# Kernel optimization log

Hardware: AMD Instinct MI355X
Metric: run time of the kernel (lower is better)

The kernel has to match this reference:

```python
import jax, jax.numpy as jnp
import numpy as np

B, DIN, H, DOUT, NC = 1024, 343, 512, 311, 4


def cubic(y0, y1, y2, y3, mu):
    # Catmull-Rom cubic interpolation (matches PFNN.cubic)
    return ((-0.5 * y0 + 1.5 * y1 - 1.5 * y2 + 0.5 * y3) * mu * mu * mu
            + (y0 - 2.5 * y1 + 2.0 * y2 - 0.5 * y3) * mu * mu
            + (-0.5 * y0 + 0.5 * y2) * mu + y1)


def setup_inputs() -> dict:
    key = jax.random.key(0)
    ks = jax.random.split(key, 7)
    s = 0.05
    x = jax.random.uniform(ks[0], (B, DIN), dtype=jnp.float32)  # phase = x[:, -1] in [0,1)
    W0 = jax.random.normal(ks[1], (NC, H, DIN - 1), dtype=jnp.float32) * s
    W1 = jax.random.normal(ks[2], (NC, H, H), dtype=jnp.float32) * s
    W2 = jax.random.normal(ks[3], (NC, DOUT, H), dtype=jnp.float32) * s
    b0 = jax.random.normal(ks[4], (NC, H), dtype=jnp.float32) * s
    b1 = jax.random.normal(ks[5], (NC, H), dtype=jnp.float32) * s
    b2 = jax.random.normal(ks[6], (NC, DOUT), dtype=jnp.float32) * s
    return {"x": x, "W0": W0, "W1": W1, "W2": W2, "b0": b0, "b1": b1, "b2": b2}


def reference(x, W0, W1, W2, b0, b1, b2):
    nc = W0.shape[0]
    phase = x[:, -1]                       # [B]
    pscale = nc * phase
    mu = jnp.mod(pscale, 1.0)              # [B]
    k1 = jnp.mod(pscale.astype(jnp.int32), nc)
    k0 = jnp.mod(k1 - 1, nc)
    k2 = jnp.mod(k1 + 1, nc)
    k3 = jnp.mod(k1 + 2, nc)
    muW = mu[:, None, None]
    mub = mu[:, None]

    def interp(P, m):
        return cubic(P[k0], P[k1], P[k2], P[k3], m)

    W0i = interp(W0, muW)  # [B, 512, DIN-1]
    W1i = interp(W1, muW)  # [B, 512, 512]
    W2i = interp(W2, muW)  # [B, DOUT, 512]
    b0i = interp(b0, mub)
    b1i = interp(b1, mub)
    b2i = interp(b2, mub)

    h0 = x[:, :-1]                                              # [B, DIN-1]
    h1 = jax.nn.elu(jnp.einsum('boi,bi->bo', W0i, h0) + b0i)    # [B, 512]
    h2 = jax.nn.elu(jnp.einsum('boi,bi->bo', W1i, h1) + b1i)    # [B, 512]
    h3 = jnp.einsum('boi,bi->bo', W2i, h2) + b2i                # [B, DOUT]
    return h3
```

## Files before the change

kernel.cpp:

```cpp
#include <hip/hip_runtime.h>
#include <math.h>

typedef short bf16x8 __attribute__((ext_vector_type(8)));
typedef float f32x16 __attribute__((ext_vector_type(16)));

__device__ __forceinline__ unsigned short f2bf(float f) {
    union { float f; unsigned u; } x; x.f = f;
    unsigned r = x.u + 0x7FFFu + ((x.u >> 16) & 1u);
    return (unsigned short)(r >> 16);
}


__global__ __launch_bounds__(256) void prep_kernel(
    const float* __restrict__ x, float* __restrict__ coef,
    unsigned short* __restrict__ xb, unsigned short* __restrict__ H1b,
    unsigned short* __restrict__ H2b)
{
    const int b = blockIdx.x, t = threadIdx.x;
    for (int k = t; k < 384; k += 256) {
        unsigned short v;
        if (k < 342)       v = f2bf(x[b * 343 + k]);
        else if (k == 342) v = 0x3F80;
        else               v = 0;
        xb[b * 384 + k] = v;
    }
    if (t >= 64 && t < 128) {
        int j = t - 64;
        H1b[b * 576 + 512 + j] = (j == 0) ? 0x3F80 : 0;
    }
    if (t >= 128 && t < 192) {
        int j = t - 128;
        H2b[b * 576 + 512 + j] = (j == 0) ? 0x3F80 : 0;
    }
    if (t == 0) {
        float phase = x[b * 343 + 342];
        float ps = 4.0f * phase;
        int k1 = (int)ps;
        float mu = ps - (float)k1;
        k1 &= 3;
        float mu2 = mu * mu, mu3 = mu2 * mu;
        float c0 = -0.5f * mu3 +        mu2 - 0.5f * mu;
        float c1 =  1.5f * mu3 - 2.5f * mu2 + 1.0f;
        float c2 = -1.5f * mu3 + 2.0f * mu2 + 0.5f * mu;
        float c3 =  0.5f * mu3 - 0.5f * mu2;
        float cc[4];
        cc[(k1 + 3) & 3] = c0;
        cc[k1]           = c1;
        cc[(k1 + 1) & 3] = c2;
        cc[(k1 + 2) & 3] = c3;
        *(float4*)(coef + b * 4) = make_float4(cc[0], cc[1], cc[2], cc[3]);
    }
}

__global__ __launch_bounds__(256) void convw_kernel(
    const float* __restrict__ W0, const float* __restrict__ W1, const float* __restrict__ W2,
    const float* __restrict__ b0, const float* __restrict__ b1, const float* __restrict__ b2,
    unsigned short* __restrict__ Wf0, unsigned short* __restrict__ Wf1, unsigned short* __restrict__ Wf2)
{
    constexpr unsigned E0 = 4u * 512 * 384;
    constexpr unsigned E1 = 4u * 512 * 576;
    constexpr unsigned E2 = 4u * 320 * 576;
    unsigned i = (blockIdx.x * 256u + threadIdx.x) * 4u;
    if (i >= E0 + E1 + E2) return;
    float v[4];
    unsigned n, o, k, NOT, NKS, KPv;
    unsigned short* dst;
    if (i < E0) {
        n = i / (512u * 384u); unsigned r = i % (512u * 384u);
        o = r / 384u; k = r % 384u; NOT = 16; NKS = 24; KPv = 384; dst = Wf0;
        unsigned row = n * 512u + o;
        #pragma unroll
        for (int j = 0; j < 4; ++j) {
            unsigned kk = k + j;
            v[j] = (kk < 342u) ? W0[(size_t)row * 342u + kk] : ((kk == 342u) ? b0[row] : 0.f);
        }
    } else if (i < E0 + E1) {
        unsigned ii = i - E0;
        n = ii / (512u * 576u); unsigned r = ii % (512u * 576u);
        o = r / 576u; k = r % 576u; NOT = 16; NKS = 36; KPv = 576; dst = Wf1;
        unsigned row = n * 512u + o;
        if (k + 3u < 512u) {
            float4 w = *(const float4*)(W1 + (size_t)row * 512u + k);
            v[0] = w.x; v[1] = w.y; v[2] = w.z; v[3] = w.w;
        } else {
            #pragma unroll
            for (int j = 0; j < 4; ++j) {
                unsigned kk = k + j;
                v[j] = (kk < 512u) ? W1[(size_t)row * 512u + kk] : ((kk == 512u) ? b1[row] : 0.f);
            }
        }
    } else {
        unsigned ii = i - E0 - E1;
        n = ii / (320u * 576u); unsigned r = ii % (320u * 576u);
        o = r / 576u; k = r % 576u; NOT = 10; NKS = 36; KPv = 576; dst = Wf2;
        v[0] = v[1] = v[2] = v[3] = 0.f;
        if (o < 311u) {
            unsigned row = n * 311u + o;
            if (k + 3u < 512u) {
                float4 w = *(const float4*)(W2 + (size_t)row * 512u + k);
                v[0] = w.x; v[1] = w.y; v[2] = w.z; v[3] = w.w;
            } else {
                #pragma unroll
                for (int j = 0; j < 4; ++j) {
                    unsigned kk = k + j;
                    v[j] = (kk < 512u) ? W2[(size_t)row * 512u + kk] : ((kk == 512u) ? b2[row] : 0.f);
                }
            }
        }
    }
    (void)KPv;
    unsigned ot = o >> 5, m = o & 31, ks = k >> 4, h = (k >> 3) & 1, j4 = k & 7;
    size_t off = (((size_t)(n * NOT + ot) * NKS + ks) * 64u + h * 32u + m) * 8u + j4;
    ushort4 pk; pk.x = f2bf(v[0]); pk.y = f2bf(v[1]); pk.z = f2bf(v[2]); pk.w = f2bf(v[3]);
    *(ushort4*)(dst + off) = pk;
}

template<bool ELU, bool OUT_BF16, int KP, int OPAD>
__global__ __launch_bounds__(256) void layer_mfma(
    const unsigned short* __restrict__ Wf,
    const unsigned short* __restrict__ Hb,
    const float* __restrict__ coef,
    unsigned short* __restrict__ HoutB,
    float* __restrict__ outF,
    int Oreal)
{
    constexpr int NOT = OPAD / 32, NKS = KP / 16, KSQ = NKS / 4, RS = KP + 8;
    __shared__ unsigned short hs[32 * RS];

    const int tid = threadIdx.x, lane = tid & 63, w = tid >> 6;
    const int ot = blockIdx.x, b0 = blockIdx.y * 32;

    constexpr int CPT = (32 * KP / 8) / 256;
    #pragma unroll
    for (int c = 0; c < CPT; ++c) {
        int idx = c * 256 + tid;
        int r = idx / (KP / 8), col = idx % (KP / 8);
        *(bf16x8*)&hs[r * RS + col * 8] = *(const bf16x8*)(Hb + (size_t)(b0 + r) * KP + col * 8);
    }
    __syncthreads();

    const int m = lane & 31, h = lane >> 5;
    const unsigned short* hrow = &hs[m * RS + h * 8 + w * KSQ * 16];
    const unsigned short* wbase = Wf + (size_t)ot * NKS * 512 + (size_t)w * KSQ * 512 + lane * 8;
    const size_t nstr = (size_t)NOT * NKS * 512;

    f32x16 acc0 = {}, acc1 = {}, acc2 = {}, acc3 = {};
    #pragma unroll
    for (int s = 0; s < KSQ; ++s) {
        bf16x8 bfr = *(const bf16x8*)(hrow + s * 16);
        bf16x8 a0 = *(const bf16x8*)(wbase + (size_t)s * 512);
        bf16x8 a1 = *(const bf16x8*)(wbase + nstr + (size_t)s * 512);
        bf16x8 a2 = *(const bf16x8*)(wbase + 2 * nstr + (size_t)s * 512);
        bf16x8 a3 = *(const bf16x8*)(wbase + 3 * nstr + (size_t)s * 512);
        acc0 = __builtin_amdgcn_mfma_f32_32x32x16_bf16(a0, bfr, acc0, 0, 0, 0);
        acc1 = __builtin_amdgcn_mfma_f32_32x32x16_bf16(a1, bfr, acc1, 0, 0, 0);
        acc2 = __builtin_amdgcn_mfma_f32_32x32x16_bf16(a2, bfr, acc2, 0, 0, 0);
        acc3 = __builtin_amdgcn_mfma_f32_32x32x16_bf16(a3, bfr, acc3, 0, 0, 0);
    }

    const int b = b0 + m;
    float4 cf = *(const float4*)(coef + b * 4);
    float sv[16];
    #pragma unroll
    for (int r = 0; r < 16; ++r)
        sv[r] = cf.x * acc0[r] + cf.y * acc1[r] + cf.z * acc2[r] + cf.w * acc3[r];

    __syncthreads();
    float* red = (float*)hs;
    if (w > 0) {
        #pragma unroll
        for (int g = 0; g < 4; ++g)
            #pragma unroll
            for (int j = 0; j < 4; ++j) {
                int row = 8 * g + 4 * h + j;
                red[(w - 1) * 1024 + row * 32 + m] = sv[g * 4 + j];
            }
    }
    __syncthreads();
    if (w == 0) {
        #pragma unroll
        for (int g = 0; g < 4; ++g) {
            float vv[4];
            #pragma unroll
            for (int j = 0; j < 4; ++j) {
                int row = 8 * g + 4 * h + j;
                float v = sv[g * 4 + j] + red[row * 32 + m]
                        + red[1024 + row * 32 + m] + red[2048 + row * 32 + m];
                if (ELU) v = (v > 0.f) ? v : expm1f(v);
                vv[j] = v;
            }
            int orow = ot * 32 + 8 * g + 4 * h;
            if (OUT_BF16) {
                ushort4 pk;
                pk.x = f2bf(vv[0]); pk.y = f2bf(vv[1]); pk.z = f2bf(vv[2]); pk.w = f2bf(vv[3]);
                *(ushort4*)(HoutB + (size_t)b * 576 + orow) = pk;
            } else {
                #pragma unroll
                for (int j = 0; j < 4; ++j)
                    if (orow + j < Oreal) outF[(size_t)b * Oreal + orow + j] = vv[j];
            }
        }
    }
}

extern "C" void kernel_launch(void* const* d_in, const int* in_sizes, int n_in,
                              void* d_out, int out_size, void* d_ws, size_t ws_size,
                              hipStream_t stream) {
    (void)in_sizes; (void)n_in; (void)out_size; (void)ws_size;
    const float* x  = (const float*)d_in[0];
    const float* W0 = (const float*)d_in[1];
    const float* W1 = (const float*)d_in[2];
    const float* W2 = (const float*)d_in[3];
    const float* b0 = (const float*)d_in[4];
    const float* b1 = (const float*)d_in[5];
    const float* b2 = (const float*)d_in[6];
    float* out = (float*)d_out;

    char* wsb = (char*)d_ws;
    float*          coef = (float*)(wsb + 0);
    unsigned short* xb   = (unsigned short*)(wsb + 16384);
    unsigned short* H1b  = (unsigned short*)(wsb + 802816);
    unsigned short* H2b  = (unsigned short*)(wsb + 1982464);
    unsigned short* Wf0  = (unsigned short*)(wsb + 3162112);
    unsigned short* Wf1  = (unsigned short*)(wsb + 4734976);
    unsigned short* Wf2  = (unsigned short*)(wsb + 7094272);

    prep_kernel<<<dim3(1024), dim3(256), 0, stream>>>(x, coef, xb, H1b, H2b);
    convw_kernel<<<dim3(2640), dim3(256), 0, stream>>>(W0, W1, W2, b0, b1, b2, Wf0, Wf1, Wf2);

    layer_mfma<true,  true,  384, 512><<<dim3(16, 32), dim3(256), 0, stream>>>(Wf0, xb,  coef, H1b, nullptr, 512);
    layer_mfma<true,  true,  576, 512><<<dim3(16, 32), dim3(256), 0, stream>>>(Wf1, H1b, coef, H2b, nullptr, 512);
    layer_mfma<false, false, 576, 320><<<dim3(10, 32), dim3(256), 0, stream>>>(Wf2, H2b, coef, nullptr, out, 311);
}
```

Baseline: 106.3 us.

## Fuse prep, weight conversion and three layers into one cooperative persistent kernel

Replaces five separate launches with a single cooperative kernel that runs input and weight conversion, then each layer, separated by grid-wide syncs. Activations are now stored directly in MFMA fragment order, so the layers read B operands from global memory without staging them in LDS. Weight conversion writes eight bf16 values per thread in fragment order. The intent is to remove launch gaps and LDS staging, at the cost of grid.sync overhead and a fixed grid of 256 or 512 blocks looping over tiles, with a multi-kernel fallback if the cooperative launch fails.

```diff
diff --git a/kernel.cpp b/kernel.cpp
--- a/kernel.cpp
+++ b/kernel.cpp
@@ -1,5 +1,8 @@
 #include <hip/hip_runtime.h>
+#include <hip/hip_cooperative_groups.h>
 #include <math.h>
+
+namespace cg = cooperative_groups;
 
 typedef short bf16x8 __attribute__((ext_vector_type(8)));
 typedef float f32x16 __attribute__((ext_vector_type(16)));
@@ -10,30 +13,33 @@
     return (unsigned short)(r >> 16);
 }
 
-
-__global__ __launch_bounds__(256) void prep_kernel(
-    const float* __restrict__ x, float* __restrict__ coef,
-    unsigned short* __restrict__ xb, unsigned short* __restrict__ H1b,
-    unsigned short* __restrict__ H2b)
+__device__ __forceinline__ bf16x8 conv8(const float* __restrict__ W,
+                                        const float* __restrict__ bias,
+                                        int row, int Kreal, int k0) {
+    bf16x8 r;
+    #pragma unroll
+    for (int j = 0; j < 8; ++j) {
+        int k = k0 + j;
+        float v = (k < Kreal) ? W[(size_t)row * Kreal + k]
+                              : ((k == Kreal) ? bias[row] : 0.f);
+        r[j] = (short)f2bf(v);
+    }
+    return r;
+}
+
+__device__ void phaseA(
+    const float* __restrict__ x,
+    const float* __restrict__ W0, const float* __restrict__ W1, const float* __restrict__ W2,
+    const float* __restrict__ bias0, const float* __restrict__ bias1, const float* __restrict__ bias2,
+    float* __restrict__ coef, unsigned short* __restrict__ xf,
+    unsigned short* __restrict__ H1f, unsigned short* __restrict__ H2f,
+    unsigned short* __restrict__ Wf0, unsigned short* __restrict__ Wf1, unsigned short* __restrict__ Wf2,
+    int bid, int tid, unsigned gsz)
 {
-    const int b = blockIdx.x, t = threadIdx.x;
-    for (int k = t; k < 384; k += 256) {
-        unsigned short v;
-        if (k < 342)       v = f2bf(x[b * 343 + k]);
-        else if (k == 342) v = 0x3F80;
-        else               v = 0;
-        xb[b * 384 + k] = v;
-    }
-    if (t >= 64 && t < 128) {
-        int j = t - 64;
-        H1b[b * 576 + 512 + j] = (j == 0) ? 0x3F80 : 0;
-    }
-    if (t >= 128 && t < 192) {
-        int j = t - 128;
-        H2b[b * 576 + 512 + j] = (j == 0) ? 0x3F80 : 0;
-    }
-    if (t == 0) {
-        float phase = x[b * 343 + 342];
+    unsigned gtid = (unsigned)bid * 256u + (unsigned)tid;
+
+    for (unsigned b = gtid; b < 1024u; b += gsz) {
+        float phase = x[b * 343u + 342u];
         float ps = 4.0f * phase;
         int k1 = (int)ps;
         float mu = ps - (float)k1;
@@ -50,157 +56,196 @@
         cc[(k1 + 2) & 3] = c3;
         *(float4*)(coef + b * 4) = make_float4(cc[0], cc[1], cc[2], cc[3]);
     }
-}
-
-__global__ __launch_bounds__(256) void convw_kernel(
-    const float* __restrict__ W0, const float* __restrict__ W1, const float* __restrict__ W2,
-    const float* __restrict__ b0, const float* __restrict__ b1, const float* __restrict__ b2,
-    unsigned short* __restrict__ Wf0, unsigned short* __restrict__ Wf1, unsigned short* __restrict__ Wf2)
-{
-    constexpr unsigned E0 = 4u * 512 * 384;
-    constexpr unsigned E1 = 4u * 512 * 576;
-    constexpr unsigned E2 = 4u * 320 * 576;
-    unsigned i = (blockIdx.x * 256u + threadIdx.x) * 4u;
-    if (i >= E0 + E1 + E2) return;
-    float v[4];
-    unsigned n, o, k, NOT, NKS, KPv;
-    unsigned short* dst;
-    if (i < E0) {
-        n = i / (512u * 384u); unsigned r = i % (512u * 384u);
-        o = r / 384u; k = r % 384u; NOT = 16; NKS = 24; KPv = 384; dst = Wf0;
-        unsigned row = n * 512u + o;
-        #pragma unroll
-        for (int j = 0; j < 4; ++j) {
-            unsigned kk = k + j;
-            v[j] = (kk < 342u) ? W0[(size_t)row * 342u + kk] : ((kk == 342u) ? b0[row] : 0.f);
-        }
-    } else if (i < E0 + E1) {
-        unsigned ii = i - E0;
-        n = ii / (512u * 576u); unsigned r = ii % (512u * 576u);
-        o = r / 576u; k = r % 576u; NOT = 16; NKS = 36; KPv = 576; dst = Wf1;
-        unsigned row = n * 512u + o;
-        if (k + 3u < 512u) {
-            float4 w = *(const float4*)(W1 + (size_t)row * 512u + k);
-            v[0] = w.x; v[1] = w.y; v[2] = w.z; v[3] = w.w;
+
+    for (unsigned c = gtid; c < 32u * 24u * 64u; c += gsz) {
+        unsigned lane = c & 63u, r = c >> 6;
+        unsigned ks = r % 24u, bt = r / 24u;
+        int b  = (int)(bt * 32u + (lane & 31u));
+        int k0 = (int)(ks * 16u + (lane >> 5) * 8u);
+        bf16x8 v;
+        #pragma unroll
+        for (int j = 0; j < 8; ++j) {
+            int k = k0 + j;
+            unsigned short s;
+            if (k < 342)       s = f2bf(x[(size_t)b * 343 + k]);
+            else if (k == 342) s = 0x3F80;
+            else               s = 0;
+            v[j] = (short)s;
+        }
+        *(bf16x8*)(xf + (size_t)c * 8) = v;
+    }
+
+    for (unsigned c = gtid; c < 32u * 4u * 64u; c += gsz) {
+        unsigned lane = c & 63u, r = c >> 6;
+        unsigned kk = r & 3u, bt = r >> 2;
+        size_t off = ((size_t)(bt * 36u + 32u + kk) * 64u + lane) * 8u;
+        bf16x8 v;
+        #pragma unroll
+        for (int j = 0; j < 8; ++j)
+            v[j] = (short)((kk == 0u && (lane >> 5) == 0u && j == 0) ? 0x3F80 : 0);
+        *(bf16x8*)(H1f + off) = v;
+        *(bf16x8*)(H2f + off) = v;
+    }
+
+    constexpr unsigned C0 = 4u * 16 * 24 * 64;
+    constexpr unsigned C1 = 4u * 16 * 36 * 64;
+    constexpr unsigned C2 = 4u * 10 * 36 * 64;
+    for (unsigned c = gtid; c < C0 + C1 + C2; c += gsz) {
+        bf16x8 v;
+        unsigned short* dst;
+        if (c < C0) {
+            unsigned lane = c & 63u, r = c >> 6, ks = r % 24u, t = r / 24u;
+            int o  = (int)((t & 15u) * 32u + (lane & 31u));
+            int k0 = (int)(ks * 16u + (lane >> 5) * 8u);
+            v = conv8(W0, bias0, (int)(t >> 4) * 512 + o, 342, k0);
+            dst = Wf0 + (size_t)c * 8;
+        } else if (c < C0 + C1) {
+            unsigned cc = c - C0;
+            unsigned lane = cc & 63u, r = cc >> 6, ks = r % 36u, t = r / 36u;
+            int o  = (int)((t & 15u) * 32u + (lane & 31u));
+            int k0 = (int)(ks * 16u + (lane >> 5) * 8u);
+            v = conv8(W1, bias1, (int)(t >> 4) * 512 + o, 512, k0);
+            dst = Wf1 + (size_t)cc * 8;
         } else {
-            #pragma unroll
-            for (int j = 0; j < 4; ++j) {
-                unsigned kk = k + j;
-                v[j] = (kk < 512u) ? W1[(size_t)row * 512u + kk] : ((kk == 512u) ? b1[row] : 0.f);
-            }
-        }
-    } else {
-        unsigned ii = i - E0 - E1;
-        n = ii / (320u * 576u); unsigned r = ii % (320u * 576u);
-        o = r / 576u; k = r % 576u; NOT = 10; NKS = 36; KPv = 576; dst = Wf2;
-        v[0] = v[1] = v[2] = v[3] = 0.f;
-        if (o < 311u) {
-            unsigned row = n * 311u + o;
-            if (k + 3u < 512u) {
-                float4 w = *(const float4*)(W2 + (size_t)row * 512u + k);
-                v[0] = w.x; v[1] = w.y; v[2] = w.z; v[3] = w.w;
+            unsigned cc = c - C0 - C1;
+            unsigned lane = cc & 63u, r = cc >> 6, ks = r % 36u, t = r / 36u;
+            unsigned ot = t % 10u, n = t / 10u;
+            int o  = (int)(ot * 32u + (lane & 31u));
+            int k0 = (int)(ks * 16u + (lane >> 5) * 8u);
+            if (o < 311) {
+                v = conv8(W2, bias2, (int)n * 311 + o, 512, k0);
             } else {
                 #pragma unroll
+                for (int j = 0; j < 8; ++j) v[j] = 0;
+            }
+            dst = Wf2 + (size_t)cc * 8;
+        }
+        *(bf16x8*)dst = v;
+    }
+}
+
+template<bool ELU, bool OUT_BF16, int KP, int OPAD>
+__device__ __forceinline__ void layer_phase(
+    const unsigned short* __restrict__ Wf,
+    const unsigned short* __restrict__ Hf,
+    const float* __restrict__ coef,
+    unsigned short* __restrict__ HoutF,
+    float* __restrict__ outF, int Oreal,
+    float* red, int bid, int tid, int gdim)
+{
+    constexpr int NOT = OPAD / 32, NKS = KP / 16, KSQ = NKS / 4;
+    const int lane = tid & 63, w = tid >> 6;
+    const int m = lane & 31, h = lane >> 5;
+    const size_t nstr = (size_t)NOT * NKS * 512;
+
+    for (int t = bid; t < NOT * 32; t += gdim) {
+        const int ot = t >> 5, bt = t & 31;
+        const unsigned short* wbase = Wf + ((size_t)ot * NKS + w * KSQ) * 512 + (size_t)lane * 8;
+        const unsigned short* bbase = Hf + ((size_t)bt * NKS + w * KSQ) * 512 + (size_t)lane * 8;
+
+        f32x16 acc0 = {}, acc1 = {}, acc2 = {}, acc3 = {};
+        #pragma unroll
+        for (int s = 0; s < KSQ; ++s) {
+            bf16x8 bfr = *(const bf16x8*)(bbase + (size_t)s * 512);
+            bf16x8 a0 = *(const bf16x8*)(wbase + (size_t)s * 512);
+            bf16x8 a1 = *(const bf16x8*)(wbase + nstr + (size_t)s * 512);
+            bf16x8 a2 = *(const bf16x8*)(wbase + 2 * nstr + (size_t)s * 512);
+            bf16x8 a3 = *(const bf16x8*)(wbase + 3 * nstr + (size_t)s * 512);
+            acc0 = __builtin_amdgcn_mfma_f32_32x32x16_bf16(a0, bfr, acc0, 0, 0, 0);
+            acc1 = __builtin_amdgcn_mfma_f32_32x32x16_bf16(a1, bfr, acc1, 0, 0, 0);
+            acc2 = __builtin_amdgcn_mfma_f32_32x32x16_bf16(a2, bfr, acc2, 0, 0, 0);
+            acc3 = __builtin_amdgcn_mfma_f32_32x32x16_bf16(a3, bfr, acc3, 0, 0, 0);
+        }
+
+        const int b = bt * 32 + m;
+        float4 cf = *(const float4*)(coef + b * 4);
+        float sv[16];
+        #pragma unroll
+        for (int r = 0; r < 16; ++r)
+            sv[r] = cf.x * acc0[r] + cf.y * acc1[r] + cf.z * acc2[r] + cf.w * acc3[r];
+
+        __syncthreads();
+        if (w > 0) {
+            #pragma unroll
+            for (int g = 0; g < 4; ++g)
+                #pragma unroll
                 for (int j = 0; j < 4; ++j) {
-                    unsigned kk = k + j;
-                    v[j] = (kk < 512u) ? W2[(size_t)row * 512u + kk] : ((kk == 512u) ? b2[row] : 0.f);
+                    int row = 8 * g + 4 * h + j;
+                    red[(w - 1) * 1024 + row * 32 + m] = sv[g * 4 + j];
+                }
+        }
+        __syncthreads();
+        if (w == 0) {
+            #pragma unroll
+            for (int g = 0; g < 4; ++g) {
+                float vv[4];
+                #pragma unroll
+                for (int j = 0; j < 4; ++j) {
+                    int row = 8 * g + 4 * h + j;
+                    float v = sv[g * 4 + j] + red[row * 32 + m]
+                            + red[1024 + row * 32 + m] + red[2048 + row * 32 + m];
+                    if (ELU) v = (v > 0.f) ? v : expm1f(v);
+                    vv[j] = v;
+                }
+                if (OUT_BF16) {
+                    size_t off = (((size_t)bt * 36 + ot * 2 + (g >> 1)) * 64
+                                  + (g & 1) * 32 + m) * 8 + 4 * h;
+                    ushort4 pk;
+                    pk.x = f2bf(vv[0]); pk.y = f2bf(vv[1]); pk.z = f2bf(vv[2]); pk.w = f2bf(vv[3]);
+                    *(ushort4*)(HoutF + off) = pk;
+                } else {
+                    int orow = ot * 32 + 8 * g + 4 * h;
+                    #pragma unroll
+                    for (int j = 0; j < 4; ++j)
+                        if (orow + j < Oreal) outF[(size_t)b * Oreal + orow + j] = vv[j];
                 }
             }
         }
     }
-    (void)KPv;
-    unsigned ot = o >> 5, m = o & 31, ks = k >> 4, h = (k >> 3) & 1, j4 = k & 7;
-    size_t off = (((size_t)(n * NOT + ot) * NKS + ks) * 64u + h * 32u + m) * 8u + j4;
-    ushort4 pk; pk.x = f2bf(v[0]); pk.y = f2bf(v[1]); pk.z = f2bf(v[2]); pk.w = f2bf(v[3]);
-    *(ushort4*)(dst + off) = pk;
-}
-
-template<bool ELU, bool OUT_BF16, int KP, int OPAD>
-__global__ __launch_bounds__(256) void layer_mfma(
-    const unsigned short* __restrict__ Wf,
-    const unsigned short* __restrict__ Hb,
-    const float* __restrict__ coef,
-    unsigned short* __restrict__ HoutB,
-    float* __restrict__ outF,
-    int Oreal)
-{
-    constexpr int NOT = OPAD / 32, NKS = KP / 16, KSQ = NKS / 4, RS = KP + 8;
-    __shared__ unsigned short hs[32 * RS];
-
-    const int tid = threadIdx.x, lane = tid & 63, w = tid >> 6;
-    const int ot = blockIdx.x, b0 = blockIdx.y * 32;
-
-    constexpr int CPT = (32 * KP / 8) / 256;
-    #pragma unroll
-    for (int c = 0; c < CPT; ++c) {
-        int idx = c * 256 + tid;
-        int r = idx / (KP / 8), col = idx % (KP / 8);
-        *(bf16x8*)&hs[r * RS + col * 8] = *(const bf16x8*)(Hb + (size_t)(b0 + r) * KP + col * 8);
-    }
-    __syncthreads();
-
-    const int m = lane & 31, h = lane >> 5;
-    const unsigned short* hrow = &hs[m * RS + h * 8 + w * KSQ * 16];
-    const unsigned short* wbase = Wf + (size_t)ot * NKS * 512 + (size_t)w * KSQ * 512 + lane * 8;
-    const size_t nstr = (size_t)NOT * NKS * 512;
-
-    f32x16 acc0 = {}, acc1 = {}, acc2 = {}, acc3 = {};
-    #pragma unroll
-    for (int s = 0; s < KSQ; ++s) {
-        bf16x8 bfr = *(const bf16x8*)(hrow + s * 16);
-        bf16x8 a0 = *(const bf16x8*)(wbase + (size_t)s * 512);
-        bf16x8 a1 = *(const bf16x8*)(wbase + nstr + (size_t)s * 512);
-        bf16x8 a2 = *(const bf16x8*)(wbase + 2 * nstr + (size_t)s * 512);
-        bf16x8 a3 = *(const bf16x8*)(wbase + 3 * nstr + (size_t)s * 512);
-        acc0 = __builtin_amdgcn_mfma_f32_32x32x16_bf16(a0, bfr, acc0, 0, 0, 0);
-        acc1 = __builtin_amdgcn_mfma_f32_32x32x16_bf16(a1, bfr, acc1, 0, 0, 0);
-        acc2 = __builtin_amdgcn_mfma_f32_32x32x16_bf16(a2, bfr, acc2, 0, 0, 0);
-        acc3 = __builtin_amdgcn_mfma_f32_32x32x16_bf16(a3, bfr, acc3, 0, 0, 0);
-    }
-
-    const int b = b0 + m;
-    float4 cf = *(const float4*)(coef + b * 4);
-    float sv[16];
-    #pragma unroll
-    for (int r = 0; r < 16; ++r)
-        sv[r] = cf.x * acc0[r] + cf.y * acc1[r] + cf.z * acc2[r] + cf.w * acc3[r];
-
-    __syncthreads();
-    float* red = (float*)hs;
-    if (w > 0) {
-        #pragma unroll
-        for (int g = 0; g < 4; ++g)
-            #pragma unroll
-            for (int j = 0; j < 4; ++j) {
-                int row = 8 * g + 4 * h + j;
-                red[(w - 1) * 1024 + row * 32 + m] = sv[g * 4 + j];
-            }
-    }
-    __syncthreads();
-    if (w == 0) {
-        #pragma unroll
-        for (int g = 0; g < 4; ++g) {
-            float vv[4];
-            #pragma unroll
-            for (int j = 0; j < 4; ++j) {
-                int row = 8 * g + 4 * h + j;
-                float v = sv[g * 4 + j] + red[row * 32 + m]
-                        + red[1024 + row * 32 + m] + red[2048 + row * 32 + m];
-                if (ELU) v = (v > 0.f) ? v : expm1f(v);
-                vv[j] = v;
-            }
-            int orow = ot * 32 + 8 * g + 4 * h;
-            if (OUT_BF16) {
-                ushort4 pk;
-                pk.x = f2bf(vv[0]); pk.y = f2bf(vv[1]); pk.z = f2bf(vv[2]); pk.w = f2bf(vv[3]);
-                *(ushort4*)(HoutB + (size_t)b * 576 + orow) = pk;
-            } else {
-                #pragma unroll
-                for (int j = 0; j < 4; ++j)
-                    if (orow + j < Oreal) outF[(size_t)b * Oreal + orow + j] = vv[j];
-            }
-        }
-    }
+}
+
+#define PFNN_ARGS \
+    const float* __restrict__ x, \
+    const float* __restrict__ W0, const float* __restrict__ W1, const float* __restrict__ W2, \
+    const float* __restrict__ bias0, const float* __restrict__ bias1, const float* __restrict__ bias2, \
+    float* __restrict__ outF, float* __restrict__ coef, \
+    unsigned short* __restrict__ xf, \
+    unsigned short* __restrict__ H1f, unsigned short* __restrict__ H2f, \
+    unsigned short* __restrict__ Wf0, unsigned short* __restrict__ Wf1, unsigned short* __restrict__ Wf2
+
+__global__ void __launch_bounds__(256, 2) pfnn_fused(PFNN_ARGS) {
+    __shared__ float red[3 * 1024];
+    const int bid = blockIdx.x, tid = threadIdx.x, gdim = gridDim.x;
+    cg::grid_group grid = cg::this_grid();
+
+    phaseA(x, W0, W1, W2, bias0, bias1, bias2, coef, xf, H1f, H2f, Wf0, Wf1, Wf2,
+           bid, tid, (unsigned)gdim * 256u);
+    grid.sync();
+    layer_phase<true,  true,  384, 512>(Wf0, xf,  coef, H1f, nullptr, 512, red, bid, tid, gdim);
+    grid.sync();
+    layer_phase<true,  true,  576, 512>(Wf1, H1f, coef, H2f, nullptr, 512, red, bid, tid, gdim);
+    grid.sync();
+    layer_phase<false, false, 576, 320>(Wf2, H2f, coef, nullptr, outF, 311, red, bid, tid, gdim);
+}
+
+__global__ void __launch_bounds__(256) phaseA_kernel(PFNN_ARGS) {
+    phaseA(x, W0, W1, W2, bias0, bias1, bias2, coef, xf, H1f, H2f, Wf0, Wf1, Wf2,
+           blockIdx.x, threadIdx.x, gridDim.x * 256u);
+    (void)outF;
+}
+__global__ void __launch_bounds__(256, 2) layer0_kernel(PFNN_ARGS) {
+    __shared__ float red[3 * 1024];
+    layer_phase<true,  true,  384, 512>(Wf0, xf,  coef, H1f, nullptr, 512, red, blockIdx.x, threadIdx.x, gridDim.x);
+    (void)outF;
+}
+__global__ void __launch_bounds__(256, 2) layer1_kernel(PFNN_ARGS) {
+    __shared__ float red[3 * 1024];
+    layer_phase<true,  true,  576, 512>(Wf1, H1f, coef, H2f, nullptr, 512, red, blockIdx.x, threadIdx.x, gridDim.x);
+    (void)outF;
+}
+__global__ void __launch_bounds__(256, 2) layer2_kernel(PFNN_ARGS) {
+    __shared__ float red[3 * 1024];
+    layer_phase<false, false, 576, 320>(Wf2, H2f, coef, nullptr, outF, 311, red, blockIdx.x, threadIdx.x, gridDim.x);
 }
 
 extern "C" void kernel_launch(void* const* d_in, const int* in_sizes, int n_in,
@@ -218,17 +263,32 @@
 
     char* wsb = (char*)d_ws;
     float*          coef = (float*)(wsb + 0);
-    unsigned short* xb   = (unsigned short*)(wsb + 16384);
-    unsigned short* H1b  = (unsigned short*)(wsb + 802816);
-    unsigned short* H2b  = (unsigned short*)(wsb + 1982464);
+    unsigned short* xf   = (unsigned short*)(wsb + 16384);
+    unsigned short* H1f  = (unsigned short*)(wsb + 802816);
+    unsigned short* H2f  = (unsigned short*)(wsb + 1982464);
     unsigned short* Wf0  = (unsigned short*)(wsb + 3162112);
     unsigned short* Wf1  = (unsigned short*)(wsb + 4734976);
     unsigned short* Wf2  = (unsigned short*)(wsb + 7094272);
 
-    prep_kernel<<<dim3(1024), dim3(256), 0, stream>>>(x, coef, xb, H1b, H2b);
-    convw_kernel<<<dim3(2640), dim3(256), 0, stream>>>(W0, W1, W2, b0, b1, b2, Wf0, Wf1, Wf2);
-
-    layer_mfma<true,  true,  384, 512><<<dim3(16, 32), dim3(256), 0, stream>>>(Wf0, xb,  coef, H1b, nullptr, 512);
-    layer_mfma<true,  true,  576, 512><<<dim3(16, 32), dim3(256), 0, stream>>>(Wf1, H1b, coef, H2b, nullptr, 512);
-    layer_mfma<false, false, 576, 320><<<dim3(10, 32), dim3(256), 0, stream>>>(Wf2, H2b, coef, nullptr, out, 311);
-}
+    int maxb = 0;
+    hipError_t qe = hipOccupancyMaxActiveBlocksPerMultiprocessor(
+        &maxb, (const void*)pfnn_fused, 256, 0);
+    int grid = 256;
+    if (qe == hipSuccess && maxb >= 2) grid = 512;
+
+    void* args[] = {
+        (void*)&x, (void*)&W0, (void*)&W1, (void*)&W2,
+        (void*)&b0, (void*)&b1, (void*)&b2, (void*)&out,
+        (void*)&coef, (void*)&xf, (void*)&H1f, (void*)&H2f,
+        (void*)&Wf0, (void*)&Wf1, (void*)&Wf2
+    };
+    hipError_t e = hipLaunchCooperativeKernel((const void*)pfnn_fused,
+                                              dim3(grid), dim3(256), args, 0, stream);
+    if (e != hipSuccess) {
+        (void)hipGetLastError();
+        phaseA_kernel<<<dim3(512), dim3(256), 0, stream>>>(x, W0, W1, W2, b0, b1, b2, out, coef, xf, H1f, H2f, Wf0, Wf1, Wf2);
+        layer0_kernel<<<dim3(512), dim3(256), 0, stream>>>(x, W0, W1, W2, b0, b1, b2, out, coef, xf, H1f, H2f, Wf0, Wf1, Wf2);
+        layer1_kernel<<<dim3(512), dim3(256), 0, stream>>>(x, W0, W1, W2, b0, b1, b2, out, coef, xf, H1f, H2f, Wf0, Wf1, Wf2);
+        layer2_kernel<<<dim3(320), dim3(256), 0, stream>>>(x, W0, W1, W2, b0, b1, b2, out, coef, xf, H1f, H2f, Wf0, Wf1, Wf2);
+    }
+}
```

Measured after the change: 212.1 us. 2x slower.
